# Kernel optimization log

Measured on AMD Instinct MI355X. Metric: run time of the kernel, lower is better.

The kernel has to match this reference:

```python
import jax, jax.numpy as jnp
import numpy as np

N_BITS = 8
N_LEVELS_FIX = 2 ** N_BITS - 1          # 255
CONSTRAINT = 0.8                         # module-level default; selected once at calibration
CLAMP_MIN = 1e-08


def setup_inputs() -> dict:
    key = jax.random.key(0)
    # [b, h, t, c] positive activations (log2 quantizer assumes x > 0, e.g. post-softmax)
    x = jax.random.uniform(key, (8, 12, 4096, 64), dtype=jnp.float32, minval=0.0, maxval=1.0)
    return {"x": x}


def _ste_round(v):
    # straight-through rounding: fwd = round, bwd = identity
    return v + jax.lax.stop_gradient(jnp.round(v) - v)


def reference(x):
    b, h, t, c = x.shape
    xr = jnp.transpose(x, (0, 2, 1, 3)).reshape(b, t, h * c)        # [b, t, h*c]

    # per-token max over channels
    error_ulg = xr.max(axis=2)                                      # [b, t]
    attn_sum = 1.0 / error_ulg
    eu = error_ulg[:, :, None]

    # masked small-value counts at log2 thresholds
    f32 = jnp.float32
    attn_std = ((xr < eu * 2.0 ** (-N_LEVELS_FIX)).sum(axis=2).astype(f32)
                - (xr < eu * 2.0 ** (-(N_LEVELS_FIX * 2.0 ** CONSTRAINT))).sum(axis=2).astype(f32))
    attn_std_down = ((xr < eu * 2.0 ** (-(N_LEVELS_FIX / 2.0))).sum(axis=2).astype(f32)
                     - (xr < eu * 2.0 ** (-(N_LEVELS_FIX / 2.0 * 2.0 ** CONSTRAINT))).sum(axis=2).astype(f32))

    # double sort + gather-based reindexing (torch: sort asc / desc with indices)
    inc_idx = jnp.argsort(error_ulg, axis=1)                        # [b, t]
    attn_sort_inc = jnp.take_along_axis(error_ulg, inc_idx, axis=1)
    dec_idx = inc_idx[:, ::-1]
    attn_sort_dec = attn_sort_inc[:, ::-1]

    std_tok = jnp.std(xr, axis=2, ddof=1)                           # torch unbiased std
    denom = std_tok.mean(axis=1, keepdims=True)                     # [b, 1]
    attn_sort_ = (attn_sort_dec * jnp.take_along_axis(attn_std, dec_idx, axis=1)
                  - attn_sort_inc * jnp.take_along_axis(attn_std_down, inc_idx, axis=1) * 2.0) / denom
    attn_sort_diff = (attn_sort_[:, : t // 2 - 1] > 0).astype(f32).sum(axis=1, keepdims=True)  # [b,1]

    # rank of each token (double argsort), smallest attn_sum -> rank 0
    rank = jnp.argsort(jnp.argsort(attn_sum, axis=1), axis=1)       # [b, t]

    # on=True branch assigns {n_bits+1, n_bits, n_bits-1} by rank band...
    bit_token = jnp.where(rank < attn_sort_diff, N_BITS + 1,
                          jnp.where(rank > (t - 1) - attn_sort_diff, N_BITS - 1, N_BITS))
    # ...but the original forward then unconditionally overwrites EVERY band to n_bits
    # (the three trailing bit_token[...] = self.n_bits lines cover all ranks):
    bit_token = jnp.full_like(bit_token, N_BITS)

    n_levels = (2.0 ** bit_token.astype(f32))[:, None, :, None]     # [b, 1, t, 1]

    # delta = detached per-token max (x viewed [b, 1, t, h*c], amax over dims (1,3))
    delta = jax.lax.stop_gradient(error_ulg)[:, None, :, None]      # [b, 1, t, 1]

    x4 = xr[:, None, :, :]                                          # [b, 1, t, h*c]
    ratio = jnp.maximum(x4 / delta, CLAMP_MIN)
    x_int = _ste_round(-jnp.log2(ratio))
    mask = x_int >= n_levels
    x_quant = jnp.clip(x_int / (n_levels - 1.0), 0.0, 1.0) * (n_levels - 1.0)
    x_dequant = delta * 2.0 ** (-x_quant)
    x_dequant = jnp.where(mask, 0.0, x_dequant)

    # back to [b, h, t, c]
    out = x_dequant.reshape(b, t, h, c).transpose(0, 2, 1, 3)
    return out
```

## Files before the change

kernel.cpp:

```cpp
#include <hip/hip_runtime.h>
#include <math.h>


#define BB 8
#define HH 12
#define TT 4096
#define CC 64

__global__ __launch_bounds__(192) void log2q_kernel(const float* __restrict__ x,
                                                    float* __restrict__ out) {
    const int g   = blockIdx.x;
    const int b   = g >> 12;
    const int t   = g & 4095;
    const int tid = threadIdx.x;
    const int h   = tid >> 4;
    const int c4  = (tid & 15) << 2;

    const size_t idx = (((size_t)b * HH + h) * TT + t) * CC + c4;
    const float4 xv = *reinterpret_cast<const float4*>(x + idx);

    float m = fmaxf(fmaxf(xv.x, xv.y), fmaxf(xv.z, xv.w));
#pragma unroll
    for (int off = 32; off > 0; off >>= 1)
        m = fmaxf(m, __shfl_xor(m, off));
    __shared__ float smax[3];
    const int wave = tid >> 6;
    if ((tid & 63) == 0) smax[wave] = m;
    __syncthreads();
    const float delta = fmaxf(fmaxf(smax[0], smax[1]), smax[2]);

    const float r[4] = {xv.x, xv.y, xv.z, xv.w};
    float o[4];
#pragma unroll
    for (int j = 0; j < 4; ++j) {
        const float ratio = fmaxf(r[j] / delta, 1e-8f);

        const float nv = -__log2f(ratio);
        float xi = rintf(nv);
        const float d = fabsf(nv - xi);
        if (0.5f - d < 1e-4f) {
            const float tt = (float)log((double)ratio);
            const float v2 = tt / 0x1.62e43p-1f;
            xi = rintf(-v2);
        }
        const float q = fminf(fmaxf(xi / 255.0f, 0.0f), 1.0f) * 255.0f;
        const float p = exp2f(-q);
        o[j] = (xi >= 256.0f) ? 0.0f : delta * p;
    }

    const float4 ov = {o[0], o[1], o[2], o[3]};
    *reinterpret_cast<float4*>(out + idx) = ov;
}

extern "C" void kernel_launch(void* const* d_in, const int* in_sizes, int n_in,
                              void* d_out, int out_size, void* d_ws, size_t ws_size,
                              hipStream_t stream) {
    const float* x = (const float*)d_in[0];
    float* out = (float*)d_out;
    dim3 grid(BB * TT);
    dim3 block(192);
    log2q_kernel<<<grid, block, 0, stream>>>(x, out);
}
```

Before: 38.48 us.

## Map one wavefront per token and use nontemporal vector loads/stores

```diff
diff --git a/kernel.cpp b/kernel.cpp
--- a/kernel.cpp
+++ b/kernel.cpp
@@ -6,50 +6,61 @@
 #define HH 12
 #define TT 4096
 #define CC 64
+#define HSTRIDE ((size_t)TT * CC)
 
-__global__ __launch_bounds__(192) void log2q_kernel(const float* __restrict__ x,
+typedef float vf4 __attribute__((ext_vector_type(4)));
+
+__global__ __launch_bounds__(256) void log2q_kernel(const float* __restrict__ x,
                                                     float* __restrict__ out) {
-    const int g   = blockIdx.x;
-    const int b   = g >> 12;
-    const int t   = g & 4095;
-    const int tid = threadIdx.x;
-    const int h   = tid >> 4;
-    const int c4  = (tid & 15) << 2;
+    const int wave = threadIdx.x >> 6;
+    const int lane = threadIdx.x & 63;
+    const int g    = (blockIdx.x << 2) | wave;
+    const int b    = g >> 12;
+    const int t    = g & 4095;
 
-    const size_t idx = (((size_t)b * HH + h) * TT + t) * CC + c4;
-    const float4 xv = *reinterpret_cast<const float4*>(x + idx);
+    const int hh = lane >> 4;
+    const int c4 = (lane & 15) << 2;
+    const size_t base = (size_t)b * (HH * HSTRIDE) + (size_t)t * CC + c4;
 
-    float m = fmaxf(fmaxf(xv.x, xv.y), fmaxf(xv.z, xv.w));
+    vf4 v[3];
+#pragma unroll
+    for (int k = 0; k < 3; ++k) {
+        const vf4* p = reinterpret_cast<const vf4*>(x + base + (size_t)(k * 4 + hh) * HSTRIDE);
+        v[k] = __builtin_nontemporal_load(p);
+    }
+
+    float m = fmaxf(fmaxf(fmaxf(v[0].x, v[0].y), fmaxf(v[0].z, v[0].w)),
+             fmaxf(fmaxf(fmaxf(v[1].x, v[1].y), fmaxf(v[1].z, v[1].w)),
+                   fmaxf(fmaxf(v[2].x, v[2].y), fmaxf(v[2].z, v[2].w))));
 #pragma unroll
     for (int off = 32; off > 0; off >>= 1)
         m = fmaxf(m, __shfl_xor(m, off));
-    __shared__ float smax[3];
-    const int wave = tid >> 6;
-    if ((tid & 63) == 0) smax[wave] = m;
-    __syncthreads();
-    const float delta = fmaxf(fmaxf(smax[0], smax[1]), smax[2]);
+    const float delta = m;
 
-    const float r[4] = {xv.x, xv.y, xv.z, xv.w};
-    float o[4];
 #pragma unroll
-    for (int j = 0; j < 4; ++j) {
-        const float ratio = fmaxf(r[j] / delta, 1e-8f);
+    for (int k = 0; k < 3; ++k) {
+        float r[4] = {v[k].x, v[k].y, v[k].z, v[k].w};
+        float o[4];
+#pragma unroll
+        for (int j = 0; j < 4; ++j) {
+            const float ratio = fmaxf(r[j] / delta, 1e-8f);
 
-        const float nv = -__log2f(ratio);
-        float xi = rintf(nv);
-        const float d = fabsf(nv - xi);
-        if (0.5f - d < 1e-4f) {
-            const float tt = (float)log((double)ratio);
-            const float v2 = tt / 0x1.62e43p-1f;
-            xi = rintf(-v2);
+            const float nv = -__log2f(ratio);
+            float xi = rintf(nv);
+            const float d = fabsf(nv - xi);
+            if (0.5f - d < 1e-4f) {
+                const float tt = (float)log((double)ratio);
+                const float v2 = tt / 0x1.62e43p-1f;
+                xi = rintf(-v2);
+            }
+            const float q = fminf(fmaxf(xi / 255.0f, 0.0f), 1.0f) * 255.0f;
+            const float p = exp2f(-q);
+            o[j] = (xi >= 256.0f) ? 0.0f : delta * p;
         }
-        const float q = fminf(fmaxf(xi / 255.0f, 0.0f), 1.0f) * 255.0f;
-        const float p = exp2f(-q);
-        o[j] = (xi >= 256.0f) ? 0.0f : delta * p;
+        vf4 ov = {o[0], o[1], o[2], o[3]};
+        vf4* po = reinterpret_cast<vf4*>(out + base + (size_t)(k * 4 + hh) * HSTRIDE);
+        __builtin_nontemporal_store(ov, po);
     }
-
-    const float4 ov = {o[0], o[1], o[2], o[3]};
-    *reinterpret_cast<float4*>(out + idx) = ov;
 }
 
 extern "C" void kernel_launch(void* const* d_in, const int* in_sizes, int n_in,
@@ -57,7 +68,7 @@
                               hipStream_t stream) {
     const float* x = (const float*)d_in[0];
     float* out = (float*)d_out;
-    dim3 grid(BB * TT);
-    dim3 block(192);
+    dim3 grid((BB * TT) / 4);
+    dim3 block(256);
     log2q_kernel<<<grid, block, 0, stream>>>(x, out);
 }
```

Result: slower. 39.38 us (+2.3%).
